# Performance work log

Measured on AMD Instinct MI355X. Metric: run time of the kernel, lower is better.

## Reference

```python
import jax, jax.numpy as jnp
import numpy as np

MARGIN = 0.2


def colbert_score(q, d):
    # q: (B, Q, D), d: (B, K, D) -> scalar
    sim = jnp.einsum('bqd,bkd->bqk', q, d)          # (B, Q, K)
    max_sim = jnp.max(sim, axis=2)                   # (B, Q) row-wise max over doc tokens
    return jnp.sum(max_sim)                          # sum over query tokens and batch


def setup_inputs() -> dict:
    key = jax.random.key(0)
    k1, k2, k3 = jax.random.split(key, 3)
    B, Q, K, D = 256, 256, 512, 128
    return {
        'q': jax.random.normal(k1, (B, Q, D), dtype=jnp.float32),
        'p': jax.random.normal(k2, (B, K, D), dtype=jnp.float32),
        'n': jax.random.normal(k3, (B, K, D), dtype=jnp.float32),
    }


def reference(q, p, n):
    pos_score = colbert_score(q, p)
    neg_score = colbert_score(q, n)
    loss = jax.nn.relu(MARGIN + neg_score - pos_score)
    # torch .mean() on a scalar is identity
    return loss
```

## Files before the change

### kernel.cpp

```cpp
#include <hip/hip_runtime.h>


#define MARGIN   0.2f
#define Bn       256
#define Qn       256
#define Kn       512
#define Dn       128
#define TN       32
#define NT       (Kn / TN)
#define BSTR     136
#define NTHREADS 512

typedef __attribute__((ext_vector_type(8))) short short8;
typedef __attribute__((ext_vector_type(4))) short short4v;
typedef __attribute__((ext_vector_type(4))) float f32x4;

__device__ __forceinline__ void split_trunc(float x, unsigned short& hi, unsigned short& lo) {
    unsigned int u = __float_as_uint(x);
    hi = (unsigned short)(u >> 16);
    float l = x - __uint_as_float(u & 0xFFFF0000u);
    lo = (unsigned short)(__float_as_uint(l) >> 16);
}

__global__ __launch_bounds__(NTHREADS, 4)
void colbert_pass_kernel(const float* __restrict__ qg,
                         const float* __restrict__ pg,
                         const float* __restrict__ ng,
                         double* __restrict__ sum_ws) {
    __shared__ short Bs[2][2][TN * BSTR];
    __shared__ float part[8];

    const int tid  = threadIdx.x;
    const int w    = tid >> 6;
    const int lane = tid & 63;
    const int l16  = lane & 15;
    const int quad = lane >> 4;
    const int b    = blockIdx.x;
    const int pass = blockIdx.y;

    const float* docb = (pass ? ng : pg) + (size_t)b * Kn * Dn;

    float4 pre[2];
    {
        const float4* s4 = (const float4*)docb;
#pragma unroll
        for (int k = 0; k < 2; ++k) pre[k] = s4[tid + 512 * k];
    }

    short8 Ahi[2][4], Alo[2][4];
    {
        const float* qb = qg + (size_t)b * Qn * Dn;
#pragma unroll
        for (int mi = 0; mi < 2; ++mi)
#pragma unroll
            for (int ks = 0; ks < 4; ++ks) {
                const float* src = qb + (size_t)(w * 32 + mi * 16 + l16) * Dn
                                      + ks * 32 + quad * 8;
                float4 v0 = *(const float4*)src;
                float4 v1 = *(const float4*)(src + 4);
                float x[8] = {v0.x, v0.y, v0.z, v0.w, v1.x, v1.y, v1.z, v1.w};
#pragma unroll
                for (int j = 0; j < 8; ++j) {
                    unsigned short h, l;
                    split_trunc(x[j], h, l);
                    Ahi[mi][ks][j] = (short)h;
                    Alo[mi][ks][j] = (short)l;
                }
            }
    }

    float maxv[2][4];
#pragma unroll
    for (int mi = 0; mi < 2; ++mi)
#pragma unroll
        for (int r = 0; r < 4; ++r) maxv[mi][r] = -3e38f;

    int buf = 0;
    for (int t = 0; t < NT; ++t) {
#pragma unroll
        for (int k = 0; k < 2; ++k) {
            int i   = tid + 512 * k;
            int doc = i >> 5;
            int d4  = i & 31;
            float4 v = pre[k];
            float x[4] = {v.x, v.y, v.z, v.w};
            short4v hi, lo;
#pragma unroll
            for (int j = 0; j < 4; ++j) {
                unsigned short h, l;
                split_trunc(x[j], h, l);
                hi[j] = (short)h;
                lo[j] = (short)l;
            }
            *(short4v*)&Bs[buf][0][doc * BSTR + d4 * 4] = hi;
            *(short4v*)&Bs[buf][1][doc * BSTR + d4 * 4] = lo;
        }
        __syncthreads();

        if (t + 1 < NT) {
            const float4* s4 = (const float4*)(docb + (size_t)(t + 1) * TN * Dn);
#pragma unroll
            for (int k = 0; k < 2; ++k) pre[k] = s4[tid + 512 * k];
        }

        f32x4 acc[2][2];
#pragma unroll
        for (int mi = 0; mi < 2; ++mi)
#pragma unroll
            for (int ni = 0; ni < 2; ++ni) acc[mi][ni] = (f32x4){0.f, 0.f, 0.f, 0.f};

#pragma unroll
        for (int ni = 0; ni < 2; ++ni) {
#pragma unroll
            for (int ks = 0; ks < 4; ++ks) {
                int off = (ni * 16 + l16) * BSTR + ks * 32 + quad * 8;
                short8 bh = *(const short8*)&Bs[buf][0][off];
                short8 bl = *(const short8*)&Bs[buf][1][off];
                acc[0][ni] = __builtin_amdgcn_mfma_f32_16x16x32_bf16(
                    Ahi[0][ks], bh, acc[0][ni], 0, 0, 0);
                acc[1][ni] = __builtin_amdgcn_mfma_f32_16x16x32_bf16(
                    Ahi[1][ks], bh, acc[1][ni], 0, 0, 0);
                acc[0][ni] = __builtin_amdgcn_mfma_f32_16x16x32_bf16(
                    Alo[0][ks], bh, acc[0][ni], 0, 0, 0);
                acc[1][ni] = __builtin_amdgcn_mfma_f32_16x16x32_bf16(
                    Alo[1][ks], bh, acc[1][ni], 0, 0, 0);
                acc[0][ni] = __builtin_amdgcn_mfma_f32_16x16x32_bf16(
                    Ahi[0][ks], bl, acc[0][ni], 0, 0, 0);
                acc[1][ni] = __builtin_amdgcn_mfma_f32_16x16x32_bf16(
                    Ahi[1][ks], bl, acc[1][ni], 0, 0, 0);
            }
        }

#pragma unroll
        for (int mi = 0; mi < 2; ++mi)
#pragma unroll
            for (int r = 0; r < 4; ++r)
                maxv[mi][r] = fmaxf(maxv[mi][r], fmaxf(acc[mi][0][r], acc[mi][1][r]));
        buf ^= 1;
    }

#pragma unroll
    for (int off = 1; off < 16; off <<= 1)
#pragma unroll
        for (int mi = 0; mi < 2; ++mi)
#pragma unroll
            for (int r = 0; r < 4; ++r)
                maxv[mi][r] = fmaxf(maxv[mi][r], __shfl_xor(maxv[mi][r], off));

    float s = 0.f;
#pragma unroll
    for (int mi = 0; mi < 2; ++mi)
#pragma unroll
        for (int r = 0; r < 4; ++r) s += maxv[mi][r];
    if (l16 != 0) s = 0.f;
    s += __shfl_xor(s, 16);
    s += __shfl_xor(s, 32);
    if (lane == 0) part[w] = s;
    __syncthreads();
    if (tid == 0) {
        double t = 0.0;
#pragma unroll
        for (int i = 0; i < 8; ++i) t += (double)part[i];
        atomicAdd(sum_ws, pass ? -t : t);
    }
}

__global__ void finalize_kernel(const double* __restrict__ sum_ws,
                                float* __restrict__ out) {
    out[0] = fmaxf(0.0f, MARGIN - (float)sum_ws[0]);
}

extern "C" void kernel_launch(void* const* d_in, const int* in_sizes, int n_in,
                              void* d_out, int out_size, void* d_ws, size_t ws_size,
                              hipStream_t stream) {
    const float* q = (const float*)d_in[0];
    const float* p = (const float*)d_in[1];
    const float* n = (const float*)d_in[2];
    float* out = (float*)d_out;
    double* ws = (double*)d_ws;

    hipMemsetAsync(ws, 0, sizeof(double), stream);

    colbert_pass_kernel<<<dim3(Bn, 2), NTHREADS, 0, stream>>>(q, p, n, ws);
    finalize_kernel<<<1, 1, 0, stream>>>(ws, out);
}
```

Baseline: 180.4 us.

## Deepen doc-tile prefetch to two tiles and interleave split/store with MFMA

The main loop is restructured so global loads are issued two tiles ahead into a pair of register buffers. The bf16 hi/lo split and LDS store for the next tile now sit between the two MFMA halves of the current tile, so that ALU and LDS-write work can overlap matrix-core work. This also leaves one barrier per iteration, placed at the end. In exchange it holds more registers for the extra prefetch buffer, which could affect occupancy at 512 threads with launch_bounds 4.

```diff
diff --git a/kernel.cpp b/kernel.cpp
--- a/kernel.cpp
+++ b/kernel.cpp
@@ -40,11 +40,17 @@
 
     const float* docb = (pass ? ng : pg) + (size_t)b * Kn * Dn;
 
-    float4 pre[2];
+    const int cdoc = tid >> 5;
+    const int cd4  = tid & 31;
+
+    float4 pre2[2][2];
     {
         const float4* s4 = (const float4*)docb;
 #pragma unroll
-        for (int k = 0; k < 2; ++k) pre[k] = s4[tid + 512 * k];
+        for (int k = 0; k < 2; ++k) pre2[0][k] = s4[tid + 512 * k];
+        const float4* s41 = (const float4*)(docb + (size_t)TN * Dn);
+#pragma unroll
+        for (int k = 0; k < 2; ++k) pre2[1][k] = s41[tid + 512 * k];
     }
 
     short8 Ahi[2][4], Alo[2][4];
@@ -69,65 +75,105 @@
             }
     }
 
+#pragma unroll
+    for (int k = 0; k < 2; ++k) {
+        int i   = tid + 512 * k;
+        int doc = i >> 5;
+        int d4  = i & 31;
+        float4 v = pre2[0][k];
+        float x[4] = {v.x, v.y, v.z, v.w};
+        short4v hi, lo;
+#pragma unroll
+        for (int j = 0; j < 4; ++j) {
+            unsigned short h, l;
+            split_trunc(x[j], h, l);
+            hi[j] = (short)h;
+            lo[j] = (short)l;
+        }
+        *(short4v*)&Bs[0][0][doc * BSTR + d4 * 4] = hi;
+        *(short4v*)&Bs[0][1][doc * BSTR + d4 * 4] = lo;
+    }
+    __syncthreads();
+
     float maxv[2][4];
 #pragma unroll
     for (int mi = 0; mi < 2; ++mi)
 #pragma unroll
         for (int r = 0; r < 4; ++r) maxv[mi][r] = -3e38f;
 
-    int buf = 0;
     for (int t = 0; t < NT; ++t) {
-#pragma unroll
-        for (int k = 0; k < 2; ++k) {
-            int i   = tid + 512 * k;
-            int doc = i >> 5;
-            int d4  = i & 31;
-            float4 v = pre[k];
-            float x[4] = {v.x, v.y, v.z, v.w};
-            short4v hi, lo;
-#pragma unroll
-            for (int j = 0; j < 4; ++j) {
-                unsigned short h, l;
-                split_trunc(x[j], h, l);
-                hi[j] = (short)h;
-                lo[j] = (short)l;
-            }
-            *(short4v*)&Bs[buf][0][doc * BSTR + d4 * 4] = hi;
-            *(short4v*)&Bs[buf][1][doc * BSTR + d4 * 4] = lo;
-        }
-        __syncthreads();
+        const int cur = t & 1;
+
+        if (t + 2 < NT) {
+            const float4* s4 = (const float4*)(docb + (size_t)(t + 2) * TN * Dn);
+#pragma unroll
+            for (int k = 0; k < 2; ++k) pre2[cur][k] = s4[tid + 512 * k];
+        }
+
+        f32x4 acc[2][2];
+#pragma unroll
+        for (int mi = 0; mi < 2; ++mi)
+#pragma unroll
+            for (int ni = 0; ni < 2; ++ni) acc[mi][ni] = (f32x4){0.f, 0.f, 0.f, 0.f};
+
+        {
+#pragma unroll
+            for (int ks = 0; ks < 4; ++ks) {
+                int off = l16 * BSTR + ks * 32 + quad * 8;
+                short8 bh = *(const short8*)&Bs[cur][0][off];
+                short8 bl = *(const short8*)&Bs[cur][1][off];
+                acc[0][0] = __builtin_amdgcn_mfma_f32_16x16x32_bf16(
+                    Ahi[0][ks], bh, acc[0][0], 0, 0, 0);
+                acc[1][0] = __builtin_amdgcn_mfma_f32_16x16x32_bf16(
+                    Ahi[1][ks], bh, acc[1][0], 0, 0, 0);
+                acc[0][0] = __builtin_amdgcn_mfma_f32_16x16x32_bf16(
+                    Alo[0][ks], bh, acc[0][0], 0, 0, 0);
+                acc[1][0] = __builtin_amdgcn_mfma_f32_16x16x32_bf16(
+                    Alo[1][ks], bh, acc[1][0], 0, 0, 0);
+                acc[0][0] = __builtin_amdgcn_mfma_f32_16x16x32_bf16(
+                    Ahi[0][ks], bl, acc[0][0], 0, 0, 0);
+                acc[1][0] = __builtin_amdgcn_mfma_f32_16x16x32_bf16(
+                    Ahi[1][ks], bl, acc[1][0], 0, 0, 0);
+            }
+        }
 
         if (t + 1 < NT) {
-            const float4* s4 = (const float4*)(docb + (size_t)(t + 1) * TN * Dn);
-#pragma unroll
-            for (int k = 0; k < 2; ++k) pre[k] = s4[tid + 512 * k];
-        }
-
-        f32x4 acc[2][2];
-#pragma unroll
-        for (int mi = 0; mi < 2; ++mi)
-#pragma unroll
-            for (int ni = 0; ni < 2; ++ni) acc[mi][ni] = (f32x4){0.f, 0.f, 0.f, 0.f};
-
-#pragma unroll
-        for (int ni = 0; ni < 2; ++ni) {
+#pragma unroll
+            for (int k = 0; k < 2; ++k) {
+                float4 v = pre2[(t + 1) & 1][k];
+                int doc = cdoc + 16 * k;
+                float x[4] = {v.x, v.y, v.z, v.w};
+                short4v hi, lo;
+#pragma unroll
+                for (int j = 0; j < 4; ++j) {
+                    unsigned short h, l;
+                    split_trunc(x[j], h, l);
+                    hi[j] = (short)h;
+                    lo[j] = (short)l;
+                }
+                *(short4v*)&Bs[cur ^ 1][0][doc * BSTR + cd4 * 4] = hi;
+                *(short4v*)&Bs[cur ^ 1][1][doc * BSTR + cd4 * 4] = lo;
+            }
+        }
+
+        {
 #pragma unroll
             for (int ks = 0; ks < 4; ++ks) {
-                int off = (ni * 16 + l16) * BSTR + ks * 32 + quad * 8;
-                short8 bh = *(const short8*)&Bs[buf][0][off];
-                short8 bl = *(const short8*)&Bs[buf][1][off];
-                acc[0][ni] = __builtin_amdgcn_mfma_f32_16x16x32_bf16(
-                    Ahi[0][ks], bh, acc[0][ni], 0, 0, 0);
-                acc[1][ni] = __builtin_amdgcn_mfma_f32_16x16x32_bf16(
-                    Ahi[1][ks], bh, acc[1][ni], 0, 0, 0);
-                acc[0][ni] = __builtin_amdgcn_mfma_f32_16x16x32_bf16(
-                    Alo[0][ks], bh, acc[0][ni], 0, 0, 0);
-                acc[1][ni] = __builtin_amdgcn_mfma_f32_16x16x32_bf16(
-                    Alo[1][ks], bh, acc[1][ni], 0, 0, 0);
-                acc[0][ni] = __builtin_amdgcn_mfma_f32_16x16x32_bf16(
-                    Ahi[0][ks], bl, acc[0][ni], 0, 0, 0);
-                acc[1][ni] = __builtin_amdgcn_mfma_f32_16x16x32_bf16(
-                    Ahi[1][ks], bl, acc[1][ni], 0, 0, 0);
+                int off = (16 + l16) * BSTR + ks * 32 + quad * 8;
+                short8 bh = *(const short8*)&Bs[cur][0][off];
+                short8 bl = *(const short8*)&Bs[cur][1][off];
+                acc[0][1] = __builtin_amdgcn_mfma_f32_16x16x32_bf16(
+                    Ahi[0][ks], bh, acc[0][1], 0, 0, 0);
+                acc[1][1] = __builtin_amdgcn_mfma_f32_16x16x32_bf16(
+                    Ahi[1][ks], bh, acc[1][1], 0, 0, 0);
+                acc[0][1] = __builtin_amdgcn_mfma_f32_16x16x32_bf16(
+                    Alo[0][ks], bh, acc[0][1], 0, 0, 0);
+                acc[1][1] = __builtin_amdgcn_mfma_f32_16x16x32_bf16(
+                    Alo[1][ks], bh, acc[1][1], 0, 0, 0);
+                acc[0][1] = __builtin_amdgcn_mfma_f32_16x16x32_bf16(
+                    Ahi[0][ks], bl, acc[0][1], 0, 0, 0);
+                acc[1][1] = __builtin_amdgcn_mfma_f32_16x16x32_bf16(
+                    Ahi[1][ks], bl, acc[1][1], 0, 0, 0);
             }
         }
 
@@ -136,7 +182,8 @@
 #pragma unroll
             for (int r = 0; r < 4; ++r)
                 maxv[mi][r] = fmaxf(maxv[mi][r], fmaxf(acc[mi][0][r], acc[mi][1][r]));
-        buf ^= 1;
+
+        __syncthreads();
     }
 
 #pragma unroll
```

After: 200.1 us. 10.9% more time.

## Software-pipeline doc tile staging with MFMA using two register prefetch sets

Applied to the files above, without the earlier changes.

Restructures the main loop so the next tile's bf16 split and LDS store happen between the two MFMA halves of the current tile. Two register prefetch sets fetch tiles two steps ahead, and there is one barrier per tile. The aim is to hide the conversion work and the global load latency behind matrix-core work. The cost is more live registers (two float4x2 prefetch sets) under launch bounds of 4 blocks, plus manual unrolling by two.

```diff
diff --git a/kernel.cpp b/kernel.cpp
--- a/kernel.cpp
+++ b/kernel.cpp
@@ -22,6 +22,65 @@
     lo = (unsigned short)(__float_as_uint(l) >> 16);
 }
 
+#define MFMA_PHASE(CUR, NI)                                                    \
+    {                                                                          \
+        _Pragma("unroll")                                                      \
+        for (int ks = 0; ks < 4; ++ks) {                                       \
+            int off = ((NI) * 16 + l16) * BSTR + ks * 32 + quad * 8;           \
+            short8 bh = *(const short8*)&Bs[CUR][0][off];                      \
+            short8 bl = *(const short8*)&Bs[CUR][1][off];                      \
+            acc[0][NI] = __builtin_amdgcn_mfma_f32_16x16x32_bf16(              \
+                Ahi[0][ks], bh, acc[0][NI], 0, 0, 0);                          \
+            acc[1][NI] = __builtin_amdgcn_mfma_f32_16x16x32_bf16(              \
+                Ahi[1][ks], bh, acc[1][NI], 0, 0, 0);                          \
+            acc[0][NI] = __builtin_amdgcn_mfma_f32_16x16x32_bf16(              \
+                Alo[0][ks], bh, acc[0][NI], 0, 0, 0);                          \
+            acc[1][NI] = __builtin_amdgcn_mfma_f32_16x16x32_bf16(              \
+                Alo[1][ks], bh, acc[1][NI], 0, 0, 0);                          \
+            acc[0][NI] = __builtin_amdgcn_mfma_f32_16x16x32_bf16(              \
+                Ahi[0][ks], bl, acc[0][NI], 0, 0, 0);                          \
+            acc[1][NI] = __builtin_amdgcn_mfma_f32_16x16x32_bf16(              \
+                Ahi[1][ks], bl, acc[1][NI], 0, 0, 0);                          \
+        }                                                                      \
+    }
+
+#define STAGE(PRE, DST)                                                        \
+    {                                                                          \
+        _Pragma("unroll")                                                      \
+        for (int k = 0; k < 2; ++k) {                                          \
+            float4 v = PRE[k];                                                 \
+            int doc = cdoc + 16 * k;                                           \
+            float x[4] = {v.x, v.y, v.z, v.w};                                 \
+            short4v hi, lo;                                                    \
+            _Pragma("unroll")                                                  \
+            for (int j = 0; j < 4; ++j) {                                      \
+                unsigned short h, l;                                           \
+                split_trunc(x[j], h, l);                                       \
+                hi[j] = (short)h;                                              \
+                lo[j] = (short)l;                                              \
+            }                                                                  \
+            *(short4v*)&Bs[DST][0][doc * BSTR + cd4 * 4] = hi;                 \
+            *(short4v*)&Bs[DST][1][doc * BSTR + cd4 * 4] = lo;                 \
+        }                                                                      \
+    }
+
+#define PREFETCH(PRE, T)                                                       \
+    if ((T) < NT) {                                                            \
+        const float4* s4 = (const float4*)(docb + (size_t)(T) * TN * Dn);      \
+        _Pragma("unroll")                                                      \
+        for (int k = 0; k < 2; ++k) PRE[k] = s4[tid + 512 * k];                \
+    }
+
+#define UPDATE_MAX()                                                           \
+    {                                                                          \
+        _Pragma("unroll")                                                      \
+        for (int mi = 0; mi < 2; ++mi)                                         \
+            _Pragma("unroll")                                                  \
+            for (int r = 0; r < 4; ++r)                                        \
+                maxv[mi][r] = fmaxf(maxv[mi][r],                               \
+                                    fmaxf(acc[mi][0][r], acc[mi][1][r]));      \
+    }
+
 __global__ __launch_bounds__(NTHREADS, 4)
 void colbert_pass_kernel(const float* __restrict__ qg,
                          const float* __restrict__ pg,
@@ -40,11 +99,17 @@
 
     const float* docb = (pass ? ng : pg) + (size_t)b * Kn * Dn;
 
-    float4 pre[2];
+    const int cdoc = tid >> 5;
+    const int cd4  = tid & 31;
+
+    float4 preE[2], preO[2];
     {
         const float4* s4 = (const float4*)docb;
 #pragma unroll
-        for (int k = 0; k < 2; ++k) pre[k] = s4[tid + 512 * k];
+        for (int k = 0; k < 2; ++k) preE[k] = s4[tid + 512 * k];
+        const float4* s41 = (const float4*)(docb + (size_t)TN * Dn);
+#pragma unroll
+        for (int k = 0; k < 2; ++k) preO[k] = s41[tid + 512 * k];
     }
 
     short8 Ahi[2][4], Alo[2][4];
@@ -69,74 +134,44 @@
             }
     }
 
+    STAGE(preE, 0)
+    __syncthreads();
+
     float maxv[2][4];
 #pragma unroll
     for (int mi = 0; mi < 2; ++mi)
 #pragma unroll
         for (int r = 0; r < 4; ++r) maxv[mi][r] = -3e38f;
 
-    int buf = 0;
-    for (int t = 0; t < NT; ++t) {
-#pragma unroll
-        for (int k = 0; k < 2; ++k) {
-            int i   = tid + 512 * k;
-            int doc = i >> 5;
-            int d4  = i & 31;
-            float4 v = pre[k];
-            float x[4] = {v.x, v.y, v.z, v.w};
-            short4v hi, lo;
-#pragma unroll
-            for (int j = 0; j < 4; ++j) {
-                unsigned short h, l;
-                split_trunc(x[j], h, l);
-                hi[j] = (short)h;
-                lo[j] = (short)l;
-            }
-            *(short4v*)&Bs[buf][0][doc * BSTR + d4 * 4] = hi;
-            *(short4v*)&Bs[buf][1][doc * BSTR + d4 * 4] = lo;
+    for (int t = 0; t < NT; t += 2) {
+        {
+            f32x4 acc[2][2];
+#pragma unroll
+            for (int mi = 0; mi < 2; ++mi)
+#pragma unroll
+                for (int ni = 0; ni < 2; ++ni) acc[mi][ni] = (f32x4){0.f, 0.f, 0.f, 0.f};
+
+            PREFETCH(preE, t + 2)
+            MFMA_PHASE(0, 0)
+            STAGE(preO, 1)
+            MFMA_PHASE(0, 1)
+            UPDATE_MAX()
+            __syncthreads();
         }
-        __syncthreads();
-
-        if (t + 1 < NT) {
-            const float4* s4 = (const float4*)(docb + (size_t)(t + 1) * TN * Dn);
-#pragma unroll
-            for (int k = 0; k < 2; ++k) pre[k] = s4[tid + 512 * k];
+        {
+            f32x4 acc[2][2];
+#pragma unroll
+            for (int mi = 0; mi < 2; ++mi)
+#pragma unroll
+                for (int ni = 0; ni < 2; ++ni) acc[mi][ni] = (f32x4){0.f, 0.f, 0.f, 0.f};
+
+            PREFETCH(preO, t + 3)
+            MFMA_PHASE(1, 0)
+            if (t + 2 < NT) STAGE(preE, 0)
+            MFMA_PHASE(1, 1)
+            UPDATE_MAX()
+            __syncthreads();
         }
-
-        f32x4 acc[2][2];
-#pragma unroll
-        for (int mi = 0; mi < 2; ++mi)
-#pragma unroll
-            for (int ni = 0; ni < 2; ++ni) acc[mi][ni] = (f32x4){0.f, 0.f, 0.f, 0.f};
-
-#pragma unroll
-        for (int ni = 0; ni < 2; ++ni) {
-#pragma unroll
-            for (int ks = 0; ks < 4; ++ks) {
-                int off = (ni * 16 + l16) * BSTR + ks * 32 + quad * 8;
-                short8 bh = *(const short8*)&Bs[buf][0][off];
-                short8 bl = *(const short8*)&Bs[buf][1][off];
-                acc[0][ni] = __builtin_amdgcn_mfma_f32_16x16x32_bf16(
-                    Ahi[0][ks], bh, acc[0][ni], 0, 0, 0);
-                acc[1][ni] = __builtin_amdgcn_mfma_f32_16x16x32_bf16(
-                    Ahi[1][ks], bh, acc[1][ni], 0, 0, 0);
-                acc[0][ni] = __builtin_amdgcn_mfma_f32_16x16x32_bf16(
-                    Alo[0][ks], bh, acc[0][ni], 0, 0, 0);
-                acc[1][ni] = __builtin_amdgcn_mfma_f32_16x16x32_bf16(
-                    Alo[1][ks], bh, acc[1][ni], 0, 0, 0);
-                acc[0][ni] = __builtin_amdgcn_mfma_f32_16x16x32_bf16(
-                    Ahi[0][ks], bl, acc[0][ni], 0, 0, 0);
-                acc[1][ni] = __builtin_amdgcn_mfma_f32_16x16x32_bf16(
-                    Ahi[1][ks], bl, acc[1][ni], 0, 0, 0);
-            }
-        }
-
-#pragma unroll
-        for (int mi = 0; mi < 2; ++mi)
-#pragma unroll
-            for (int r = 0; r < 4; ++r)
-                maxv[mi][r] = fmaxf(maxv[mi][r], fmaxf(acc[mi][0][r], acc[mi][1][r]));
-        buf ^= 1;
     }
 
 #pragma unroll
```

New measurement: 188.6 us. 4.6% more time.

## Split query rows across two blocks with 256-thread blocks

Applied to the files above, without the earlier changes.

Each block now handles half of a batch's query rows (128 instead of 256) with 4 waves, and the grid doubles to Bn x 4. The goal is more, smaller blocks for better occupancy and scheduling, while each doc tile is loaded and split into bf16 hi/lo twice per batch. The MFMA accumulators are also restructured per column tile, which lowers register pressure. The cost is doubled global reads and conversion of the doc tensors.

```diff
diff --git a/kernel.cpp b/kernel.cpp
--- a/kernel.cpp
+++ b/kernel.cpp
@@ -9,7 +9,7 @@
 #define TN       32
 #define NT       (Kn / TN)
 #define BSTR     136
-#define NTHREADS 512
+#define NTHREADS 256
 
 typedef __attribute__((ext_vector_type(8))) short short8;
 typedef __attribute__((ext_vector_type(4))) short short4v;
@@ -28,7 +28,7 @@
                          const float* __restrict__ ng,
                          double* __restrict__ sum_ws) {
     __shared__ short Bs[2][2][TN * BSTR];
-    __shared__ float part[8];
+    __shared__ float part[4];
 
     const int tid  = threadIdx.x;
     const int w    = tid >> 6;
@@ -36,15 +36,17 @@
     const int l16  = lane & 15;
     const int quad = lane >> 4;
     const int b    = blockIdx.x;
-    const int pass = blockIdx.y;
+    const int y    = blockIdx.y;
+    const int pass = y >> 1;
+    const int qh   = y & 1;
 
     const float* docb = (pass ? ng : pg) + (size_t)b * Kn * Dn;
 
-    float4 pre[2];
+    float4 pre[4];
     {
         const float4* s4 = (const float4*)docb;
 #pragma unroll
-        for (int k = 0; k < 2; ++k) pre[k] = s4[tid + 512 * k];
+        for (int k = 0; k < 4; ++k) pre[k] = s4[tid + 256 * k];
     }
 
     short8 Ahi[2][4], Alo[2][4];
@@ -54,7 +56,7 @@
         for (int mi = 0; mi < 2; ++mi)
 #pragma unroll
             for (int ks = 0; ks < 4; ++ks) {
-                const float* src = qb + (size_t)(w * 32 + mi * 16 + l16) * Dn
+                const float* src = qb + (size_t)(qh * 128 + w * 32 + mi * 16 + l16) * Dn
                                       + ks * 32 + quad * 8;
                 float4 v0 = *(const float4*)src;
                 float4 v1 = *(const float4*)(src + 4);
@@ -78,8 +80,8 @@
     int buf = 0;
     for (int t = 0; t < NT; ++t) {
 #pragma unroll
-        for (int k = 0; k < 2; ++k) {
-            int i   = tid + 512 * k;
+        for (int k = 0; k < 4; ++k) {
+            int i   = tid + 256 * k;
             int doc = i >> 5;
             int d4  = i & 31;
             float4 v = pre[k];
@@ -100,42 +102,31 @@
         if (t + 1 < NT) {
             const float4* s4 = (const float4*)(docb + (size_t)(t + 1) * TN * Dn);
 #pragma unroll
-            for (int k = 0; k < 2; ++k) pre[k] = s4[tid + 512 * k];
+            for (int k = 0; k < 4; ++k) pre[k] = s4[tid + 256 * k];
         }
-
-        f32x4 acc[2][2];
-#pragma unroll
-        for (int mi = 0; mi < 2; ++mi)
-#pragma unroll
-            for (int ni = 0; ni < 2; ++ni) acc[mi][ni] = (f32x4){0.f, 0.f, 0.f, 0.f};
 
 #pragma unroll
         for (int ni = 0; ni < 2; ++ni) {
+            f32x4 a0 = (f32x4){0.f, 0.f, 0.f, 0.f};
+            f32x4 a1 = (f32x4){0.f, 0.f, 0.f, 0.f};
 #pragma unroll
             for (int ks = 0; ks < 4; ++ks) {
                 int off = (ni * 16 + l16) * BSTR + ks * 32 + quad * 8;
                 short8 bh = *(const short8*)&Bs[buf][0][off];
                 short8 bl = *(const short8*)&Bs[buf][1][off];
-                acc[0][ni] = __builtin_amdgcn_mfma_f32_16x16x32_bf16(
-                    Ahi[0][ks], bh, acc[0][ni], 0, 0, 0);
-                acc[1][ni] = __builtin_amdgcn_mfma_f32_16x16x32_bf16(
-                    Ahi[1][ks], bh, acc[1][ni], 0, 0, 0);
-                acc[0][ni] = __builtin_amdgcn_mfma_f32_16x16x32_bf16(
-                    Alo[0][ks], bh, acc[0][ni], 0, 0, 0);
-                acc[1][ni] = __builtin_amdgcn_mfma_f32_16x16x32_bf16(
-                    Alo[1][ks], bh, acc[1][ni], 0, 0, 0);
-                acc[0][ni] = __builtin_amdgcn_mfma_f32_16x16x32_bf16(
-                    Ahi[0][ks], bl, acc[0][ni], 0, 0, 0);
-                acc[1][ni] = __builtin_amdgcn_mfma_f32_16x16x32_bf16(
-                    Ahi[1][ks], bl, acc[1][ni], 0, 0, 0);
+                a0 = __builtin_amdgcn_mfma_f32_16x16x32_bf16(Ahi[0][ks], bh, a0, 0, 0, 0);
+                a1 = __builtin_amdgcn_mfma_f32_16x16x32_bf16(Ahi[1][ks], bh, a1, 0, 0, 0);
+                a0 = __builtin_amdgcn_mfma_f32_16x16x32_bf16(Alo[0][ks], bh, a0, 0, 0, 0);
+                a1 = __builtin_amdgcn_mfma_f32_16x16x32_bf16(Alo[1][ks], bh, a1, 0, 0, 0);
+                a0 = __builtin_amdgcn_mfma_f32_16x16x32_bf16(Ahi[0][ks], bl, a0, 0, 0, 0);
+                a1 = __builtin_amdgcn_mfma_f32_16x16x32_bf16(Ahi[1][ks], bl, a1, 0, 0, 0);
+            }
+#pragma unroll
+            for (int r = 0; r < 4; ++r) {
+                maxv[0][r] = fmaxf(maxv[0][r], a0[r]);
+                maxv[1][r] = fmaxf(maxv[1][r], a1[r]);
             }
         }
-
-#pragma unroll
-        for (int mi = 0; mi < 2; ++mi)
-#pragma unroll
-            for (int r = 0; r < 4; ++r)
-                maxv[mi][r] = fmaxf(maxv[mi][r], fmaxf(acc[mi][0][r], acc[mi][1][r]));
         buf ^= 1;
     }
 
@@ -158,9 +149,7 @@
     if (lane == 0) part[w] = s;
     __syncthreads();
     if (tid == 0) {
-        double t = 0.0;
-#pragma unroll
-        for (int i = 0; i < 8; ++i) t += (double)part[i];
+        double t = (double)part[0] + part[1] + part[2] + part[3];
         atomicAdd(sum_ws, pass ? -t : t);
     }
 }
@@ -181,6 +170,6 @@
 
     hipMemsetAsync(ws, 0, sizeof(double), stream);
 
-    colbert_pass_kernel<<<dim3(Bn, 2), NTHREADS, 0, stream>>>(q, p, n, ws);
+    colbert_pass_kernel<<<dim3(Bn, 4), NTHREADS, 0, stream>>>(q, p, n, ws);
     finalize_kernel<<<1, 1, 0, stream>>>(ws, out);
 }
```

Measured after the change: 182.0 us. Within noise of the previous version (+0.9%).
